# Kernel tuning notes

Measured on AMD Instinct MI355X. Metric: run time of the kernel, lower is better.

The kernel has to match this reference:

```python
import jax, jax.numpy as jnp
import numpy as np

B, T, D, H, L = 32, 2048, 256, 256, 2  # batch, seq, input, hidden, layers


def setup_inputs() -> dict:
    key = jax.random.key(0)
    ks = jax.random.split(key, 5)
    s = 1.0 / np.sqrt(H)  # torch GRU uniform(-1/sqrt(H), 1/sqrt(H)) scale
    return {
        "x": jax.random.normal(ks[0], (B, T, D), dtype=jnp.float32),
        "W_ih": jax.random.uniform(ks[1], (L, 3 * H, D), jnp.float32, -s, s),
        "W_hh": jax.random.uniform(ks[2], (L, 3 * H, H), jnp.float32, -s, s),
        "b_ih": jax.random.uniform(ks[3], (L, 3 * H), jnp.float32, -s, s),
        "b_hh": jax.random.uniform(ks[4], (L, 3 * H), jnp.float32, -s, s),
    }


def _gru_layer(x_btd, W_ih_l, W_hh_l, b_ih_l, b_hh_l, h0_bh):
    # Precompute input projections for the whole sequence: [B,T,3H]
    x_proj = jnp.einsum("btd,gd->btg", x_btd, W_ih_l) + b_ih_l
    x_proj_t = jnp.swapaxes(x_proj, 0, 1)  # [T,B,3H] for scan over time

    def step(h, xp):
        hp = h @ W_hh_l.T + b_hh_l  # [B,3H]
        xr, xz, xn = jnp.split(xp, 3, axis=-1)
        hr, hz, hn = jnp.split(hp, 3, axis=-1)
        r = jax.nn.sigmoid(xr + hr)
        z = jax.nn.sigmoid(xz + hz)
        n = jnp.tanh(xn + r * hn)
        h_new = (1.0 - z) * n + z * h
        return h_new, h_new

    _, ys = jax.lax.scan(step, h0_bh, x_proj_t)  # ys: [T,B,H]
    return jnp.swapaxes(ys, 0, 1)  # [B,T,H]


def reference(x, W_ih, W_hh, b_ih, b_hh):
    # h0 = ones, matching the torch module's hidden_0 = ones(...)
    h0 = jnp.ones((x.shape[0], H), dtype=x.dtype)
    out = x
    for l in range(L):  # small fixed layer count
        out = _gru_layer(out, W_ih[l], W_hh[l], b_ih[l], b_hh[l], h0)
    return out
```

## Files before the change

kernel.cpp:

```cpp
#include <hip/hip_runtime.h>

typedef _Float16 h2 __attribute__((ext_vector_type(2)));
typedef _Float16 h8 __attribute__((ext_vector_type(8)));
typedef float f4 __attribute__((ext_vector_type(4)));

__global__ void cvt_f32_f16(const float* __restrict__ s, _Float16* __restrict__ d, int n) {
    int i = blockIdx.x * blockDim.x + threadIdx.x;
    if (i < n) d[i] = (_Float16)s[i];
}

template<bool AF16>
__global__ __launch_bounds__(256, 2) void gemm_xproj(
    const void* __restrict__ Ap, const _Float16* __restrict__ Bt,
    const float* __restrict__ bias, float* __restrict__ C)
{
    __shared__ __align__(16) _Float16 As[128 * 40];
    __shared__ __align__(16) _Float16 Bs[128 * 40];
    const int tid = threadIdx.x;
    const size_t m0 = (size_t)blockIdx.x * 128;
    const int n0 = blockIdx.y * 128;
    const int lane = tid & 63, wave = tid >> 6;
    const int wm = wave >> 1, wn = wave & 1;
    const int r16 = lane & 15, kg = lane >> 4;
    f4 acc[4][4] = {};
    for (int k0 = 0; k0 < 256; k0 += 32) {
        if (k0) __syncthreads();
        #pragma unroll
        for (int u = 0; u < 2; ++u) {
            int c = tid + u * 256;
            int row = c >> 2, off = (c & 3) * 8;
            h8 av;
            if constexpr (AF16) {
                av = *(const h8*)((const _Float16*)Ap + (m0 + row) * 256 + k0 + off);
            } else {
                const float* ap = (const float*)Ap + (m0 + row) * 256 + k0 + off;
                f4 f0 = *(const f4*)ap, f1 = *(const f4*)(ap + 4);
                av[0]=(_Float16)f0[0]; av[1]=(_Float16)f0[1]; av[2]=(_Float16)f0[2]; av[3]=(_Float16)f0[3];
                av[4]=(_Float16)f1[0]; av[5]=(_Float16)f1[1]; av[6]=(_Float16)f1[2]; av[7]=(_Float16)f1[3];
            }
            *(h8*)&As[row * 40 + off] = av;
            h8 bv = *(const h8*)(Bt + (size_t)(n0 + row) * 256 + k0 + off);
            *(h8*)&Bs[row * 40 + off] = bv;
        }
        __syncthreads();
        h8 af[4], bf[4];
        #pragma unroll
        for (int mi = 0; mi < 4; ++mi) af[mi] = *(const h8*)&As[(wm*64 + mi*16 + r16) * 40 + kg * 8];
        #pragma unroll
        for (int ni = 0; ni < 4; ++ni) bf[ni] = *(const h8*)&Bs[(wn*64 + ni*16 + r16) * 40 + kg * 8];
        #pragma unroll
        for (int mi = 0; mi < 4; ++mi)
            #pragma unroll
            for (int ni = 0; ni < 4; ++ni)
                acc[mi][ni] = __builtin_amdgcn_mfma_f32_16x16x32_f16(af[mi], bf[ni], acc[mi][ni], 0, 0, 0);
    }
    #pragma unroll
    for (int mi = 0; mi < 4; ++mi)
        #pragma unroll
        for (int ni = 0; ni < 4; ++ni) {
            int col = n0 + wn*64 + ni*16 + r16;
            float bv = bias[col];
            #pragma unroll
            for (int r = 0; r < 4; ++r) {
                int row = wm*64 + mi*16 + kg*4 + r;
                C[(m0 + row) * 768 + col] = acc[mi][ni][r] + bv;
            }
        }
}

template<bool OUTF32>
__global__ __launch_bounds__(512, 2) void gru_scan(
    const float* __restrict__ xp,
    const _Float16* __restrict__ Whh,
    const float* __restrict__ bhh,
    float* __restrict__ o32,
    _Float16* __restrict__ o16)
{
    __shared__ __align__(16) _Float16 hh[2][2][160];
    const int b = blockIdx.x;
    const int tid = threadIdx.x;
    const int j = tid >> 1, hlf = tid & 1;

    int4 w4[3][16];
    {
        const _Float16* base = Whh + (size_t)j * 256 + hlf * 128;
        #pragma unroll
        for (int g = 0; g < 3; ++g) {
            const int4* p = (const int4*)(base + (size_t)g * 256 * 256);
            #pragma unroll
            for (int k8 = 0; k8 < 16; ++k8) {
                const int4* q = p + k8;
                asm volatile("global_load_dwordx4 %0, %1, off" : "=v"(w4[g][k8]) : "v"(q));
            }
        }
        asm volatile("s_waitcnt vmcnt(0)" ::: "memory");
        __builtin_amdgcn_sched_barrier(0);
    }
    const float br = bhh[j], bz = bhh[j + 256], bn = bhh[j + 512];
    if (tid < 256) hh[0][tid >> 7][tid & 127] = (_Float16)1.0f;
    float hprev = 1.0f;
    __syncthreads();

    const float* xb = xp + (size_t)b * 2048 * 768;
    float xr0 = xb[j],       xz0 = xb[j + 256],       xn0 = xb[j + 512];
    float xr1 = xb[768 + j], xz1 = xb[768 + j + 256], xn1 = xb[768 + j + 512];
    int cur = 0;
    for (int t = 0; t < 2048; ++t) {
        const int tn = (t + 2 < 2048) ? t + 2 : 2047;
        const float* xnx = xb + (size_t)tn * 768;
        float pr = xnx[j], pz = xnx[j + 256], pn = xnx[j + 512];

        float ar0 = 0.f, ar1 = 0.f, az0 = 0.f, az1 = 0.f, an0 = 0.f, an1 = 0.f;
        const h8* hv8 = (const h8*)&hh[cur][hlf][0];
        #pragma unroll
        for (int k8 = 0; k8 < 16; ++k8) {
            h8 hc = hv8[k8];
            h2 hp[4]; __builtin_memcpy(&hp, &hc, 16);
            int4 vr = w4[0][k8], vz = w4[1][k8], vn = w4[2][k8];
            ar0 = __builtin_amdgcn_fdot2(__builtin_bit_cast(h2, vr.x), hp[0], ar0, false);
            ar1 = __builtin_amdgcn_fdot2(__builtin_bit_cast(h2, vr.y), hp[1], ar1, false);
            az0 = __builtin_amdgcn_fdot2(__builtin_bit_cast(h2, vz.x), hp[0], az0, false);
            az1 = __builtin_amdgcn_fdot2(__builtin_bit_cast(h2, vz.y), hp[1], az1, false);
            an0 = __builtin_amdgcn_fdot2(__builtin_bit_cast(h2, vn.x), hp[0], an0, false);
            an1 = __builtin_amdgcn_fdot2(__builtin_bit_cast(h2, vn.y), hp[1], an1, false);
            ar0 = __builtin_amdgcn_fdot2(__builtin_bit_cast(h2, vr.z), hp[2], ar0, false);
            ar1 = __builtin_amdgcn_fdot2(__builtin_bit_cast(h2, vr.w), hp[3], ar1, false);
            az0 = __builtin_amdgcn_fdot2(__builtin_bit_cast(h2, vz.z), hp[2], az0, false);
            az1 = __builtin_amdgcn_fdot2(__builtin_bit_cast(h2, vz.w), hp[3], az1, false);
            an0 = __builtin_amdgcn_fdot2(__builtin_bit_cast(h2, vn.z), hp[2], an0, false);
            an1 = __builtin_amdgcn_fdot2(__builtin_bit_cast(h2, vn.w), hp[3], an1, false);
        }
        float ar = ar0 + ar1, az = az0 + az1, an = an0 + an1;
        ar += __shfl_xor(ar, 1);
        az += __shfl_xor(az, 1);
        an += __shfl_xor(an, 1);

        float rg = 1.f / (1.f + __expf(-(xr0 + ar + br)));
        float zg = 1.f / (1.f + __expf(-(xz0 + az + bz)));
        float narg = xn0 + rg * (an + bn);
        float aa = fabsf(narg);
        float e = __expf(-2.f * aa);
        float ng = copysignf((1.f - e) / (1.f + e), narg);
        float hnew = (1.f - zg) * ng + zg * hprev;
        hprev = hnew;

        const int nxt = cur ^ 1;
        if (hlf == 0) {
            hh[nxt][j >> 7][j & 127] = (_Float16)hnew;
            size_t oi = ((size_t)b * 2048 + t) * 256 + j;
            if constexpr (OUTF32) o32[oi] = hnew; else o16[oi] = (_Float16)hnew;
        }
        __syncthreads();
        cur = nxt;
        xr0 = xr1; xz0 = xz1; xn0 = xn1;
        xr1 = pr;  xz1 = pz;  xn1 = pn;
    }
}

extern "C" void kernel_launch(void* const* d_in, const int* in_sizes, int n_in,
                              void* d_out, int out_size, void* d_ws, size_t ws_size,
                              hipStream_t stream) {
    const float* x    = (const float*)d_in[0];
    const float* W_ih = (const float*)d_in[1];
    const float* W_hh = (const float*)d_in[2];
    const float* b_ih = (const float*)d_in[3];
    const float* b_hh = (const float*)d_in[4];
    float* out = (float*)d_out;

    char* ws = (char*)d_ws;
    float*     xproj = (float*)ws;
    _Float16*  Wih_h = (_Float16*)(ws + 201326592);
    _Float16*  Whh_h = (_Float16*)(ws + 201326592 + 786432);
    _Float16*  y1h   = (_Float16*)(ws + 201326592 + 2 * 786432);

    cvt_f32_f16<<<1536, 256, 0, stream>>>(W_ih, Wih_h, 393216);
    cvt_f32_f16<<<1536, 256, 0, stream>>>(W_hh, Whh_h, 393216);

    gemm_xproj<false><<<dim3(512, 6), 256, 0, stream>>>(x, Wih_h, b_ih, xproj);
    gru_scan<false><<<32, 512, 0, stream>>>(xproj, Whh_h, b_hh, nullptr, y1h);

    gemm_xproj<true><<<dim3(512, 6), 256, 0, stream>>>(y1h, Wih_h + 196608, b_ih + 768, xproj);
    gru_scan<true><<<32, 512, 0, stream>>>(xproj, Whh_h + 196608, b_hh + 768, out, nullptr);
}
```

Before: 5.309 ms.

## Split GRU recurrent dot products across four threads per hidden unit

The recurrent scan now uses 1024 threads per block, so each hidden unit's W_hh row is split across four threads (64 columns each) instead of two. Per-thread serial fdot2 work per step is halved, and weights held in registers drop from 48 to 24 int4. The cost is a two-level shuffle reduction and a 1024-thread barrier every timestep, and the gate math now runs only on one lane in four. The inline-asm weight loads were also replaced with plain loads.

```diff
diff --git a/kernel.cpp b/kernel.cpp
--- a/kernel.cpp
+++ b/kernel.cpp
@@ -69,91 +69,90 @@
 }
 
 template<bool OUTF32>
-__global__ __launch_bounds__(512, 2) void gru_scan(
+__global__ __launch_bounds__(1024) void gru_scan(
     const float* __restrict__ xp,
     const _Float16* __restrict__ Whh,
     const float* __restrict__ bhh,
     float* __restrict__ o32,
     _Float16* __restrict__ o16)
 {
-    __shared__ __align__(16) _Float16 hh[2][2][160];
+    __shared__ __align__(16) _Float16 hh[2][4][72];
     const int b = blockIdx.x;
     const int tid = threadIdx.x;
-    const int j = tid >> 1, hlf = tid & 1;
+    const int j = tid >> 2, kq = tid & 3;
 
-    int4 w4[3][16];
+    int4 w4[3][8];
     {
-        const _Float16* base = Whh + (size_t)j * 256 + hlf * 128;
+        const _Float16* base = Whh + (size_t)j * 256 + kq * 64;
         #pragma unroll
         for (int g = 0; g < 3; ++g) {
             const int4* p = (const int4*)(base + (size_t)g * 256 * 256);
             #pragma unroll
-            for (int k8 = 0; k8 < 16; ++k8) {
-                const int4* q = p + k8;
-                asm volatile("global_load_dwordx4 %0, %1, off" : "=v"(w4[g][k8]) : "v"(q));
-            }
+            for (int k8 = 0; k8 < 8; ++k8) w4[g][k8] = p[k8];
         }
-        asm volatile("s_waitcnt vmcnt(0)" ::: "memory");
-        __builtin_amdgcn_sched_barrier(0);
     }
     const float br = bhh[j], bz = bhh[j + 256], bn = bhh[j + 512];
-    if (tid < 256) hh[0][tid >> 7][tid & 127] = (_Float16)1.0f;
+    if (tid < 256) hh[0][tid >> 6][tid & 63] = (_Float16)1.0f;
     float hprev = 1.0f;
     __syncthreads();
 
     const float* xb = xp + (size_t)b * 2048 * 768;
-    float xr0 = xb[j],       xz0 = xb[j + 256],       xn0 = xb[j + 512];
-    float xr1 = xb[768 + j], xz1 = xb[768 + j + 256], xn1 = xb[768 + j + 512];
+    float xr0 = 0.f, xz0 = 0.f, xn0 = 0.f, xr1 = 0.f, xz1 = 0.f, xn1 = 0.f;
+    if (kq == 0) {
+        xr0 = xb[j];       xz0 = xb[j + 256];       xn0 = xb[j + 512];
+        xr1 = xb[768 + j]; xz1 = xb[768 + j + 256]; xn1 = xb[768 + j + 512];
+    }
     int cur = 0;
     for (int t = 0; t < 2048; ++t) {
-        const int tn = (t + 2 < 2048) ? t + 2 : 2047;
-        const float* xnx = xb + (size_t)tn * 768;
-        float pr = xnx[j], pz = xnx[j + 256], pn = xnx[j + 512];
+        float pr = 0.f, pz = 0.f, pn = 0.f;
+        if (kq == 0) {
+            const int tn = (t + 2 < 2048) ? t + 2 : 2047;
+            const float* xnx = xb + (size_t)tn * 768;
+            pr = xnx[j]; pz = xnx[j + 256]; pn = xnx[j + 512];
+        }
 
-        float ar0 = 0.f, ar1 = 0.f, az0 = 0.f, az1 = 0.f, an0 = 0.f, an1 = 0.f;
-        const h8* hv8 = (const h8*)&hh[cur][hlf][0];
+        float ar = 0.f, az = 0.f, an = 0.f;
+        const h8* hseg = (const h8*)&hh[cur][kq][0];
         #pragma unroll
-        for (int k8 = 0; k8 < 16; ++k8) {
-            h8 hc = hv8[k8];
+        for (int k8 = 0; k8 < 8; ++k8) {
+            h8 hc = hseg[k8];
             h2 hp[4]; __builtin_memcpy(&hp, &hc, 16);
             int4 vr = w4[0][k8], vz = w4[1][k8], vn = w4[2][k8];
-            ar0 = __builtin_amdgcn_fdot2(__builtin_bit_cast(h2, vr.x), hp[0], ar0, false);
-            ar1 = __builtin_amdgcn_fdot2(__builtin_bit_cast(h2, vr.y), hp[1], ar1, false);
-            az0 = __builtin_amdgcn_fdot2(__builtin_bit_cast(h2, vz.x), hp[0], az0, false);
-            az1 = __builtin_amdgcn_fdot2(__builtin_bit_cast(h2, vz.y), hp[1], az1, false);
-            an0 = __builtin_amdgcn_fdot2(__builtin_bit_cast(h2, vn.x), hp[0], an0, false);
-            an1 = __builtin_amdgcn_fdot2(__builtin_bit_cast(h2, vn.y), hp[1], an1, false);
-            ar0 = __builtin_amdgcn_fdot2(__builtin_bit_cast(h2, vr.z), hp[2], ar0, false);
-            ar1 = __builtin_amdgcn_fdot2(__builtin_bit_cast(h2, vr.w), hp[3], ar1, false);
-            az0 = __builtin_amdgcn_fdot2(__builtin_bit_cast(h2, vz.z), hp[2], az0, false);
-            az1 = __builtin_amdgcn_fdot2(__builtin_bit_cast(h2, vz.w), hp[3], az1, false);
-            an0 = __builtin_amdgcn_fdot2(__builtin_bit_cast(h2, vn.z), hp[2], an0, false);
-            an1 = __builtin_amdgcn_fdot2(__builtin_bit_cast(h2, vn.w), hp[3], an1, false);
+            ar = __builtin_amdgcn_fdot2(__builtin_bit_cast(h2, vr.x), hp[0], ar, false);
+            az = __builtin_amdgcn_fdot2(__builtin_bit_cast(h2, vz.x), hp[0], az, false);
+            an = __builtin_amdgcn_fdot2(__builtin_bit_cast(h2, vn.x), hp[0], an, false);
+            ar = __builtin_amdgcn_fdot2(__builtin_bit_cast(h2, vr.y), hp[1], ar, false);
+            az = __builtin_amdgcn_fdot2(__builtin_bit_cast(h2, vz.y), hp[1], az, false);
+            an = __builtin_amdgcn_fdot2(__builtin_bit_cast(h2, vn.y), hp[1], an, false);
+            ar = __builtin_amdgcn_fdot2(__builtin_bit_cast(h2, vr.z), hp[2], ar, false);
+            az = __builtin_amdgcn_fdot2(__builtin_bit_cast(h2, vz.z), hp[2], az, false);
+            an = __builtin_amdgcn_fdot2(__builtin_bit_cast(h2, vn.z), hp[2], an, false);
+            ar = __builtin_amdgcn_fdot2(__builtin_bit_cast(h2, vr.w), hp[3], ar, false);
+            az = __builtin_amdgcn_fdot2(__builtin_bit_cast(h2, vz.w), hp[3], az, false);
+            an = __builtin_amdgcn_fdot2(__builtin_bit_cast(h2, vn.w), hp[3], an, false);
         }
-        float ar = ar0 + ar1, az = az0 + az1, an = an0 + an1;
-        ar += __shfl_xor(ar, 1);
-        az += __shfl_xor(az, 1);
-        an += __shfl_xor(an, 1);
-
-        float rg = 1.f / (1.f + __expf(-(xr0 + ar + br)));
-        float zg = 1.f / (1.f + __expf(-(xz0 + az + bz)));
-        float narg = xn0 + rg * (an + bn);
-        float aa = fabsf(narg);
-        float e = __expf(-2.f * aa);
-        float ng = copysignf((1.f - e) / (1.f + e), narg);
-        float hnew = (1.f - zg) * ng + zg * hprev;
-        hprev = hnew;
+        ar += __shfl_xor(ar, 1); ar += __shfl_xor(ar, 2);
+        az += __shfl_xor(az, 1); az += __shfl_xor(az, 2);
+        an += __shfl_xor(an, 1); an += __shfl_xor(an, 2);
 
         const int nxt = cur ^ 1;
-        if (hlf == 0) {
-            hh[nxt][j >> 7][j & 127] = (_Float16)hnew;
+        if (kq == 0) {
+            float rg = 1.f / (1.f + __expf(-(xr0 + ar + br)));
+            float zg = 1.f / (1.f + __expf(-(xz0 + az + bz)));
+            float narg = xn0 + rg * (an + bn);
+            float aa = fabsf(narg);
+            float e = __expf(-2.f * aa);
+            float ng = copysignf((1.f - e) / (1.f + e), narg);
+            float hnew = (1.f - zg) * ng + zg * hprev;
+            hprev = hnew;
+            hh[nxt][j >> 6][j & 63] = (_Float16)hnew;
             size_t oi = ((size_t)b * 2048 + t) * 256 + j;
             if constexpr (OUTF32) o32[oi] = hnew; else o16[oi] = (_Float16)hnew;
+            xr0 = xr1; xz0 = xz1; xn0 = xn1;
+            xr1 = pr;  xz1 = pz;  xn1 = pn;
         }
         __syncthreads();
         cur = nxt;
-        xr0 = xr1; xz0 = xz1; xn0 = xn1;
-        xr1 = pr;  xz1 = pz;  xn1 = pn;
     }
 }
 
@@ -177,8 +176,8 @@
     cvt_f32_f16<<<1536, 256, 0, stream>>>(W_hh, Whh_h, 393216);
 
     gemm_xproj<false><<<dim3(512, 6), 256, 0, stream>>>(x, Wih_h, b_ih, xproj);
-    gru_scan<false><<<32, 512, 0, stream>>>(xproj, Whh_h, b_hh, nullptr, y1h);
+    gru_scan<false><<<32, 1024, 0, stream>>>(xproj, Whh_h, b_hh, nullptr, y1h);
 
     gemm_xproj<true><<<dim3(512, 6), 256, 0, stream>>>(y1h, Wih_h + 196608, b_ih + 768, xproj);
-    gru_scan<true><<<32, 512, 0, stream>>>(xproj, Whh_h + 196608, b_hh + 768, out, nullptr);
+    gru_scan<true><<<32, 1024, 0, stream>>>(xproj, Whh_h + 196608, b_hh + 768, out, nullptr);
 }
```

Measured after the change: 9.427 ms. 77.6% more time.
